# Kernel optimization log

Hardware: AMD Instinct MI355X
Metric: run time of the kernel (lower is better)

The kernel has to match this reference:

```python
import jax, jax.numpy as jnp
import numpy as np

HIDDEN = 768
HEADS = 12
HEAD_DIM = HIDDEN // HEADS
DEPTH = 8
B, S = 4, 512


def setup_inputs() -> dict:
    key = jax.random.key(0)
    ks = jax.random.split(key, 12)
    sc = 0.02
    return {
        "hidden_states": jax.random.normal(ks[0], (B, S, HIDDEN), dtype=jnp.float32),
        "attention_mask": jnp.ones((B, S), dtype=jnp.int32),
        "Wq": jax.random.normal(ks[1], (HIDDEN, HIDDEN), dtype=jnp.float32) * sc,
        "bq": jnp.zeros((HIDDEN,), dtype=jnp.float32),
        "Wk": jax.random.normal(ks[2], (HIDDEN, HIDDEN), dtype=jnp.float32) * sc,
        "bk": jnp.zeros((HIDDEN,), dtype=jnp.float32),
        "Wv": jax.random.normal(ks[3], (HIDDEN, HIDDEN), dtype=jnp.float32) * sc,
        "bv": jnp.zeros((HIDDEN,), dtype=jnp.float32),
        "Wqd": jax.random.normal(ks[4], (HIDDEN * DEPTH, HIDDEN), dtype=jnp.float32) * sc,
        "bqd": jnp.zeros((HIDDEN * DEPTH,), dtype=jnp.float32),
        "Wkd": jax.random.normal(ks[5], (HIDDEN * DEPTH, HIDDEN), dtype=jnp.float32) * sc,
        "bkd": jnp.zeros((HIDDEN * DEPTH,), dtype=jnp.float32),
    }


def reference(hidden_states, attention_mask, Wq, bq, Wk, bk, Wv, bv, Wqd, bqd, Wkd, bkd):
    b, s, _ = hidden_states.shape
    # projections (nn.Linear: x @ W.T + b)
    V = (hidden_states @ Wv.T + bv).reshape(b, s, HEADS, HEAD_DIM).transpose(0, 2, 1, 3)  # [B,H,S,hd]
    Qd = (hidden_states @ Wqd.T + bqd).reshape(b, s, HEADS, HEAD_DIM, DEPTH).transpose(0, 2, 1, 3, 4)  # [B,H,S,hd,D]
    Kd = (hidden_states @ Wkd.T + bkd).reshape(b, s, HEADS, HEAD_DIM, DEPTH).transpose(0, 2, 1, 3, 4)
    # per-depth QK^T scores: [B,H,Sq,Sk,D]
    scores = jnp.einsum('bhqed,bhked->bhqkd', Qd, Kd) / np.sqrt(HEAD_DIM).astype(np.float32)
    # mask broadcasts over the key axis: [B,1,1,S,1]
    mask = attention_mask[:, None, None, :, None]
    scores = jnp.where(mask == 0, jnp.float32(-1e9), scores)
    # softmax over key dim (axis=-2 of [B,H,Sq,Sk,D])
    weights = jax.nn.softmax(scores, axis=3)
    # per-depth AV matmul, stacked on leading depth axis: [D,B,H,S,hd]
    depth_outputs = jnp.einsum('bhqkd,bhke->dbhqe', weights, V)
    return depth_outputs
```

## Files before the change

kernel.cpp:

```cpp
#include <hip/hip_runtime.h>

#define HIDDEN 768
#define HEADS 12
#define HEAD_DIM 64
#define DEPTH 8
#define BB 4
#define SS 512
#define MM (BB * SS)
#define NQD (HIDDEN * DEPTH)

typedef __bf16 bf16x8 __attribute__((ext_vector_type(8)));
typedef float f32x4 __attribute__((ext_vector_type(4)));
typedef float f32x16 __attribute__((ext_vector_type(16)));
typedef unsigned short u16x8 __attribute__((ext_vector_type(8)));

static __device__ __forceinline__ unsigned short f2bf(float f) {
  union { float f; unsigned u; } c; c.f = f;
  unsigned u = c.u;
  u = u + 0x7fffu + ((u >> 16) & 1u);
  return (unsigned short)(u >> 16);
}

static __device__ __forceinline__ unsigned cvt_pk_bf16(float lo, float hi) {
  unsigned r;
  asm("v_cvt_pk_bf16_f32 %0, %1, %2" : "=v"(r) : "v"(lo), "v"(hi));
  return r;
}

static __device__ __forceinline__ void gld16(const void* g, void* l) {
  __builtin_amdgcn_global_load_lds((const __attribute__((address_space(1))) void*)g,
                                   (__attribute__((address_space(3))) void*)l, 16, 0, 0);
}

__global__ void convert2_f32_bf16(const float* __restrict__ s0, unsigned short* __restrict__ d0,
                                  int n4_0, const float* __restrict__ s1,
                                  unsigned short* __restrict__ d1, int n4_1) {
  int i = blockIdx.x * blockDim.x + threadIdx.x;
  const float* src; unsigned short* dst; int j;
  if (i < n4_0) { src = s0; dst = d0; j = i; }
  else { j = i - n4_0; if (j >= n4_1) return; src = s1; dst = d1; }
  float4 v = reinterpret_cast<const float4*>(src)[j];
  ushort4 o;
  o.x = f2bf(v.x); o.y = f2bf(v.y); o.z = f2bf(v.z); o.w = f2bf(v.w);
  reinterpret_cast<ushort4*>(dst)[j] = o;
}

__global__ void convert_w_perm2(const float* __restrict__ s0, const float* __restrict__ s1,
                                unsigned short* __restrict__ dst, int n4each) {
  int i = blockIdx.x * blockDim.x + threadIdx.x;
  const float* src = s0; unsigned short* d = dst; int j = i;
  if (i >= n4each) {
    j = i - n4each;
    if (j >= n4each) return;
    src = s1; d = dst + (size_t)NQD * HIDDEN;
  }
  int row = j / 192;
  int cg  = j - row * 192;
  int nr = (row & ~511) | ((row & 7) << 6) | ((row >> 3) & 63);
  float4 v = reinterpret_cast<const float4*>(src)[j];
  ushort4 o;
  o.x = f2bf(v.x); o.y = f2bf(v.y); o.z = f2bf(v.z); o.w = f2bf(v.w);
  reinterpret_cast<ushort4*>(&d[(size_t)nr * HIDDEN])[cg] = o;
}

__global__ void convert_bias_perm2(const float* __restrict__ s0, const float* __restrict__ s1,
                                   float* __restrict__ dst, int n) {
  int i = blockIdx.x * blockDim.x + threadIdx.x;
  const float* src = s0; float* d = dst; int j = i;
  if (i >= n) {
    j = i - n;
    if (j >= n) return;
    src = s1; d = dst + n;
  }
  int nr = (j & ~511) | ((j & 7) << 6) | ((j >> 3) & 63);
  d[nr] = src[j];
}

__global__ __launch_bounds__(256) void gemm_bt(
    const unsigned short* __restrict__ A, const unsigned short* __restrict__ W,
    const float* __restrict__ bias, unsigned short* __restrict__ out0,
    unsigned short* __restrict__ out1, int K, int mode) {
  __shared__ unsigned short At[2][4096];
  __shared__ unsigned short Bt[2][4096];
  const int tid = threadIdx.x;
  const int nwg = gridDim.x * gridDim.y;
  const int orig = blockIdx.y * gridDim.x + blockIdx.x;
  const int wg = (orig & 7) * (nwg >> 3) + (orig >> 3);
  const int bm = (wg % gridDim.x) * 128;
  const int bn = (wg / gridDim.x) * 128;
  const int wave = tid >> 6, lane = tid & 63;
  const int wm = (wave >> 1) * 64, wn = (wave & 1) * 64;
  const int lg = lane >> 4, lr = lane & 15;
  const int srow = tid >> 2, scol = (tid & 3) * 8;
  f32x4 acc[4][4] = {};
  const unsigned short* aptr = A + (size_t)(bm + srow) * K + scol;
  const unsigned short* wptr = W + (size_t)(bn + srow) * K + scol;

  auto stage = [&](int buf, int k0) {
    gld16(aptr + k0,                  &At[buf][tid * 8]);
    gld16(aptr + (size_t)64 * K + k0, &At[buf][2048 + tid * 8]);
    gld16(wptr + k0,                  &Bt[buf][tid * 8]);
    gld16(wptr + (size_t)64 * K + k0, &Bt[buf][2048 + tid * 8]);
  };

  stage(0, 0);
  __syncthreads();

  int cur = 0;
  for (int k0 = 32; k0 <= K; k0 += 32) {
    if (k0 < K) stage(cur ^ 1, k0);
    bf16x8 af[4], bfr[4];
#pragma unroll
    for (int mi = 0; mi < 4; ++mi)
      af[mi] = *reinterpret_cast<const bf16x8*>(&At[cur][(wm + mi * 16 + lr) * 32 + lg * 8]);
#pragma unroll
    for (int ni = 0; ni < 4; ++ni)
      bfr[ni] = *reinterpret_cast<const bf16x8*>(&Bt[cur][(wn + ni * 16 + lr) * 32 + lg * 8]);
#pragma unroll
    for (int mi = 0; mi < 4; ++mi)
#pragma unroll
      for (int ni = 0; ni < 4; ++ni)
        acc[mi][ni] = __builtin_amdgcn_mfma_f32_16x16x32_bf16(af[mi], bfr[ni], acc[mi][ni], 0, 0, 0);
    __syncthreads();
    cur ^= 1;
  }

  unsigned short* outp = out0;
  float scale = 1.0f;
  int nbase = 0;
  if (mode == 1 && bn >= NQD) { outp = out1; nbase = NQD; }
  else if (mode == 1) { scale = 0.125f; }
#pragma unroll
  for (int mi = 0; mi < 4; ++mi)
#pragma unroll
    for (int ni = 0; ni < 4; ++ni)
#pragma unroll
      for (int i = 0; i < 4; ++i) {
        int m = bm + wm + mi * 16 + lg * 4 + i;
        int n = bn + wn + ni * 16 + lr;
        float v = acc[mi][ni][i];
        size_t addr;
        if (mode == 0) {
          v = (v + bias[m]);
          addr = ((size_t)((n >> 9) * 12 + (m >> 6)) * 64 + (size_t)(m & 63)) * 512 + (size_t)(n & 511);
        } else {
          v = (v + bias[n]) * scale;
          int nr = n - nbase;
          addr = ((size_t)(((m >> 9) * 12 + (nr >> 9)) * 8 + ((nr >> 6) & 7)) * 512 + (size_t)(m & 511)) * 64 + (size_t)(nr & 63);
        }
        outp[addr] = f2bf(v);
      }
}

__global__ __launch_bounds__(256) void attn32(
    const unsigned short* __restrict__ Qd, const unsigned short* __restrict__ Kd,
    const unsigned short* __restrict__ Vt, const int* __restrict__ mask,
    float* __restrict__ out) {
  __shared__ unsigned char KsB[64 * 128];
  __shared__ unsigned char VsB[64 * 128];
  __shared__ float mLds[64];
  __shared__ int mflag;
  const int tid = threadIdx.x;
  const int bid = blockIdx.x;
  const int qt = bid & 3;
  const int inst = bid >> 2;
  const int bh = inst >> 3;
  const int b = bh / 12;
  const int wave = tid >> 6, lane = tid & 63;
  const int l31 = lane & 31, hi = lane >> 5;
  const size_t qkbase = (size_t)inst * (SS * 64);
  const size_t vbase = (size_t)bh * (64 * SS);

  if (tid == 0) mflag = 0;
  __syncthreads();
  {
    int m0 = mask[b * SS + tid], m1 = mask[b * SS + 256 + tid];
    if ((m0 == 0) || (m1 == 0)) mflag = 1;
  }
  __syncthreads();
  const bool hasmask = (mflag != 0);

  const int q0w = qt * 128 + wave * 32;
  bf16x8 aq[4];
  {
    const unsigned short* qrow = Qd + qkbase + (size_t)(q0w + l31) * 64 + 8 * hi;
#pragma unroll
    for (int s = 0; s < 4; ++s)
      aq[s] = *reinterpret_cast<const bf16x8*>(qrow + 16 * s);
  }

  const int sr = tid >> 3;
  const int sc = (tid & 7) * 8;
  const int swz_lo = sr * 128 + ((sc * 2) ^ ((sr & 7) << 4));
  const int swz_hi = (sr + 32) * 128 + ((sc * 2) ^ (((sr + 32) & 7) << 4));

  f32x16 o[2] = {};
  float psum = 0.f;

  u16x8 rk0 = *reinterpret_cast<const u16x8*>(&Kd[qkbase + (size_t)sr * 64 + sc]);
  u16x8 rk1 = *reinterpret_cast<const u16x8*>(&Kd[qkbase + (size_t)(sr + 32) * 64 + sc]);
  u16x8 rv0 = *reinterpret_cast<const u16x8*>(&Vt[vbase + (size_t)sr * SS + sc]);
  u16x8 rv1 = *reinterpret_cast<const u16x8*>(&Vt[vbase + (size_t)(sr + 32) * SS + sc]);

  for (int t = 0; t < SS / 64; ++t) {
    *reinterpret_cast<u16x8*>(KsB + swz_lo) = rk0;
    *reinterpret_cast<u16x8*>(KsB + swz_hi) = rk1;
    *reinterpret_cast<u16x8*>(VsB + swz_lo) = rv0;
    *reinterpret_cast<u16x8*>(VsB + swz_hi) = rv1;
    if (hasmask && tid < 64) mLds[tid] = mask[b * SS + t * 64 + tid] ? 0.f : -1e9f;
    __syncthreads();

    if (t < SS / 64 - 1) {
      const int kn = (t + 1) * 64;
      rk0 = *reinterpret_cast<const u16x8*>(&Kd[qkbase + (size_t)(kn + sr) * 64 + sc]);
      rk1 = *reinterpret_cast<const u16x8*>(&Kd[qkbase + (size_t)(kn + sr + 32) * 64 + sc]);
      rv0 = *reinterpret_cast<const u16x8*>(&Vt[vbase + (size_t)sr * SS + kn + sc]);
      rv1 = *reinterpret_cast<const u16x8*>(&Vt[vbase + (size_t)(sr + 32) * SS + kn + sc]);
    }

    f32x16 st[2];
#pragma unroll
    for (int kh = 0; kh < 2; ++kh) {
      f32x16 acc = {};
      const int row = kh * 32 + l31;
      const int rswz = (row & 7) << 4;
#pragma unroll
      for (int s = 0; s < 4; ++s) {
        bf16x8 ak = *reinterpret_cast<const bf16x8*>(KsB + row * 128 + ((32 * s + 16 * hi) ^ rswz));
        acc = __builtin_amdgcn_mfma_f32_32x32x16_bf16(ak, aq[s], acc, 0, 0, 0);
      }
      st[kh] = acc;
    }

    if (hasmask) {
#pragma unroll
      for (int h = 0; h < 2; ++h)
#pragma unroll
        for (int r = 0; r < 16; ++r)
          st[h][r] += mLds[32 * h + (r & 3) + 8 * (r >> 2) + 4 * hi];
    }

    float pv[2][16];
#pragma unroll
    for (int h = 0; h < 2; ++h)
#pragma unroll
      for (int r = 0; r < 16; ++r) {
        float p = __expf(st[h][r]);
        psum += p;
        pv[h][r] = p;
      }

#pragma unroll
    for (int ks = 0; ks < 4; ++ks) {
      const int h = ks >> 1, rb = 8 * (ks & 1);
      unsigned w0 = cvt_pk_bf16(pv[h][rb + 0], pv[h][rb + 1]);
      unsigned w1 = cvt_pk_bf16(pv[h][rb + 2], pv[h][rb + 3]);
      unsigned w2 = cvt_pk_bf16(pv[h][rb + 4], pv[h][rb + 5]);
      unsigned w3 = cvt_pk_bf16(pv[h][rb + 6], pv[h][rb + 7]);
      asm("v_permlane32_swap_b32 %0, %1" : "+v"(w0), "+v"(w2));
      asm("v_permlane32_swap_b32 %0, %1" : "+v"(w1), "+v"(w3));
      union { unsigned u[4]; bf16x8 v; } pa;
      pa.u[0] = w0; pa.u[1] = w1; pa.u[2] = w2; pa.u[3] = w3;
#pragma unroll
      for (int et = 0; et < 2; ++et) {
        const int vrow = 32 * et + l31;
        bf16x8 bv = *reinterpret_cast<const bf16x8*>(
            VsB + vrow * 128 + ((32 * ks + 16 * hi) ^ ((vrow & 7) << 4)));
        o[et] = __builtin_amdgcn_mfma_f32_32x32x16_bf16(pa.v, bv, o[et], 0, 0, 0);
      }
    }
    __syncthreads();
  }

  psum += __shfl_xor(psum, 32);
  float inv = 1.f / psum;
  float iv[16];
#pragma unroll
  for (int r = 0; r < 16; ++r)
    iv[r] = __shfl(inv, (r & 3) + 8 * (r >> 2) + 4 * hi);

  const int d = inst & 7;
  const int hh = bh % 12;
  const size_t obase = (((size_t)d * BB + b) * HEADS + hh) * (SS * 64);
#pragma unroll
  for (int et = 0; et < 2; ++et)
#pragma unroll
    for (int r = 0; r < 16; ++r) {
      const int qrow = (r & 3) + 8 * (r >> 2) + 4 * hi;
      out[obase + (size_t)(q0w + qrow) * 64 + 32 * et + l31] = o[et][r] * iv[r];
    }
}

extern "C" void kernel_launch(void* const* d_in, const int* in_sizes, int n_in,
                              void* d_out, int out_size, void* d_ws, size_t ws_size,
                              hipStream_t stream) {
  const float* hs  = (const float*)d_in[0];
  const int* mask  = (const int*)d_in[1];
  const float* Wv  = (const float*)d_in[6];
  const float* bv  = (const float*)d_in[7];
  const float* Wqd = (const float*)d_in[8];
  const float* bqd = (const float*)d_in[9];
  const float* Wkd = (const float*)d_in[10];
  const float* bkd = (const float*)d_in[11];

  char* ws = (char*)d_ws;
  unsigned short* A_bf   = (unsigned short*)ws; ws += (size_t)MM * HIDDEN * 2;
  unsigned short* Wv_bf  = (unsigned short*)ws; ws += (size_t)HIDDEN * HIDDEN * 2;
  unsigned short* Wqk_bf = (unsigned short*)ws; ws += (size_t)(2 * NQD) * HIDDEN * 2;
  float*          bqk_p  = (float*)ws;          ws += (size_t)(2 * NQD) * 4;
  unsigned short* Qd     = (unsigned short*)ws; ws += (size_t)MM * NQD * 2;
  unsigned short* Kd     = (unsigned short*)ws; ws += (size_t)MM * NQD * 2;
  unsigned short* Vt     = (unsigned short*)ws; ws += (size_t)MM * HIDDEN * 2;

  {
    int a4 = MM * HIDDEN / 4, b4 = HIDDEN * HIDDEN / 4;
    convert2_f32_bf16<<<(a4 + b4 + 255) / 256, 256, 0, stream>>>(hs, A_bf, a4, Wv, Wv_bf, b4);
  }
  {
    int n4 = NQD * HIDDEN / 4;
    convert_w_perm2<<<(2 * n4 + 255) / 256, 256, 0, stream>>>(Wqd, Wkd, Wqk_bf, n4);
    convert_bias_perm2<<<(2 * NQD + 255) / 256, 256, 0, stream>>>(bqd, bkd, bqk_p, NQD);
  }

  gemm_bt<<<dim3(HIDDEN / 128, MM / 128), 256, 0, stream>>>(
      Wv_bf, A_bf, bv, Vt, nullptr, HIDDEN, 0);
  gemm_bt<<<dim3(MM / 128, 2 * NQD / 128), 256, 0, stream>>>(
      A_bf, Wqk_bf, bqk_p, Qd, Kd, HIDDEN, 1);

  attn32<<<BB * HEADS * DEPTH * (SS / 128), 256, 0, stream>>>(Qd, Kd, Vt, mask, (float*)d_out);
}
```

Baseline: 159.2 us.

## Add 256x256-tile QK projection GEMM with swizzled LDS and 8 waves

```diff
diff --git a/kernel.cpp b/kernel.cpp
--- a/kernel.cpp
+++ b/kernel.cpp
@@ -78,8 +78,7 @@
 
 __global__ __launch_bounds__(256) void gemm_bt(
     const unsigned short* __restrict__ A, const unsigned short* __restrict__ W,
-    const float* __restrict__ bias, unsigned short* __restrict__ out0,
-    unsigned short* __restrict__ out1, int K, int mode) {
+    const float* __restrict__ bias, unsigned short* __restrict__ out0, int K) {
   __shared__ unsigned short At[2][4096];
   __shared__ unsigned short Bt[2][4096];
   const int tid = threadIdx.x;
@@ -125,11 +124,6 @@
     cur ^= 1;
   }
 
-  unsigned short* outp = out0;
-  float scale = 1.0f;
-  int nbase = 0;
-  if (mode == 1 && bn >= NQD) { outp = out1; nbase = NQD; }
-  else if (mode == 1) { scale = 0.125f; }
 #pragma unroll
   for (int mi = 0; mi < 4; ++mi)
 #pragma unroll
@@ -138,16 +132,88 @@
       for (int i = 0; i < 4; ++i) {
         int m = bm + wm + mi * 16 + lg * 4 + i;
         int n = bn + wn + ni * 16 + lr;
-        float v = acc[mi][ni][i];
-        size_t addr;
-        if (mode == 0) {
-          v = (v + bias[m]);
-          addr = ((size_t)((n >> 9) * 12 + (m >> 6)) * 64 + (size_t)(m & 63)) * 512 + (size_t)(n & 511);
-        } else {
-          v = (v + bias[n]) * scale;
-          int nr = n - nbase;
-          addr = ((size_t)(((m >> 9) * 12 + (nr >> 9)) * 8 + ((nr >> 6) & 7)) * 512 + (size_t)(m & 511)) * 64 + (size_t)(nr & 63);
-        }
+        float v = acc[mi][ni][i] + bias[m];
+        size_t addr = ((size_t)((n >> 9) * 12 + (m >> 6)) * 64 + (size_t)(m & 63)) * 512 + (size_t)(n & 511);
+        out0[addr] = f2bf(v);
+      }
+}
+
+__global__ __launch_bounds__(512, 2) void gemm_qk256(
+    const unsigned short* __restrict__ A, const unsigned short* __restrict__ W,
+    const float* __restrict__ bias, unsigned short* __restrict__ out0,
+    unsigned short* __restrict__ out1, int K) {
+  __shared__ unsigned short At[2][8192];
+  __shared__ unsigned short Bt[2][8192];
+  const int tid = threadIdx.x;
+  const int nwg = gridDim.x * gridDim.y;
+  const int orig = blockIdx.y * gridDim.x + blockIdx.x;
+  const int wg = (orig & 7) * (nwg >> 3) + (orig >> 3);
+  const int bm = (wg % gridDim.x) * 256;
+  const int bn = (wg / gridDim.x) * 256;
+  const int wave = tid >> 6, lane = tid & 63;
+  const int wr = wave >> 2, wc = wave & 3;
+  const int lg = lane >> 4, lr = lane & 15;
+
+  const int tr = tid >> 2;
+  const int cb = (tid & 3) * 16;
+  const int colel = (cb ^ (((tr >> 1) & 3) << 4)) >> 1;
+  const unsigned short* srcA = A + (size_t)(bm + tr) * K + colel;
+  const unsigned short* srcW = W + (size_t)(bn + tr) * K + colel;
+
+  f32x4 acc[8][4] = {};
+
+  auto stage = [&](int buf, int k0) {
+    gld16(srcA + k0,                   &At[buf][tid * 8]);
+    gld16(srcA + (size_t)128 * K + k0, &At[buf][4096 + tid * 8]);
+    gld16(srcW + k0,                   &Bt[buf][tid * 8]);
+    gld16(srcW + (size_t)128 * K + k0, &Bt[buf][4096 + tid * 8]);
+  };
+
+  stage(0, 0);
+  __syncthreads();
+
+  const int rdswz = ((((lr >> 1) & 3) ^ lg) << 4);
+
+  int cur = 0;
+  for (int k0 = 32; k0 <= K; k0 += 32) {
+    if (k0 < K) stage(cur ^ 1, k0);
+    bf16x8 af[8], bfr[4];
+    const char* abase = (const char*)&At[cur][0];
+    const char* bbase = (const char*)&Bt[cur][0];
+#pragma unroll
+    for (int mi = 0; mi < 8; ++mi) {
+      const int row = wr * 128 + mi * 16 + lr;
+      af[mi] = *reinterpret_cast<const bf16x8*>(abase + row * 64 + rdswz);
+    }
+#pragma unroll
+    for (int ni = 0; ni < 4; ++ni) {
+      const int row = wc * 64 + ni * 16 + lr;
+      bfr[ni] = *reinterpret_cast<const bf16x8*>(bbase + row * 64 + rdswz);
+    }
+#pragma unroll
+    for (int mi = 0; mi < 8; ++mi)
+#pragma unroll
+      for (int ni = 0; ni < 4; ++ni)
+        acc[mi][ni] = __builtin_amdgcn_mfma_f32_16x16x32_bf16(af[mi], bfr[ni], acc[mi][ni], 0, 0, 0);
+    __syncthreads();
+    cur ^= 1;
+  }
+
+  unsigned short* outp = out0;
+  int nbase = 0;
+  float scale = 0.125f;
+  if (bn >= NQD) { outp = out1; nbase = NQD; scale = 1.0f; }
+#pragma unroll
+  for (int mi = 0; mi < 8; ++mi)
+#pragma unroll
+    for (int ni = 0; ni < 4; ++ni)
+#pragma unroll
+      for (int i = 0; i < 4; ++i) {
+        int m = bm + wr * 128 + mi * 16 + lg * 4 + i;
+        int n = bn + wc * 64 + ni * 16 + lr;
+        float v = (acc[mi][ni][i] + bias[n]) * scale;
+        int nr = n - nbase;
+        size_t addr = ((size_t)(((m >> 9) * 12 + (nr >> 9)) * 8 + ((nr >> 6) & 7)) * 512 + (size_t)(m & 511)) * 64 + (size_t)(nr & 63);
         outp[addr] = f2bf(v);
       }
 }
@@ -323,9 +389,9 @@
   }
 
   gemm_bt<<<dim3(HIDDEN / 128, MM / 128), 256, 0, stream>>>(
-      Wv_bf, A_bf, bv, Vt, nullptr, HIDDEN, 0);
-  gemm_bt<<<dim3(MM / 128, 2 * NQD / 128), 256, 0, stream>>>(
-      A_bf, Wqk_bf, bqk_p, Qd, Kd, HIDDEN, 1);
+      Wv_bf, A_bf, bv, Vt, HIDDEN);
+  gemm_qk256<<<dim3(MM / 256, 2 * NQD / 256), 512, 0, stream>>>(
+      A_bf, Wqk_bf, bqk_p, Qd, Kd, HIDDEN);
 
   attn32<<<BB * HEADS * DEPTH * (SS / 128), 256, 0, stream>>>(Qd, Kd, Vt, mask, (float*)d_out);
 }
```

Measured after the change: 148.3 us. 6.8% less time.
